# Kernel optimization log

Measured on AMD Instinct MI355X. Metric: run time of the kernel, lower is better.

## Reference

```python
import jax, jax.numpy as jnp
import numpy as np

NUM_EMBEDDINGS = 8192
EMBEDDING_DIM = 256
COMMITMENT_COST = 0.25


def setup_inputs() -> dict:
    key = jax.random.key(0)
    k1, k2 = jax.random.split(key)
    inputs = jax.random.normal(k1, (32, 32, 32, EMBEDDING_DIM), dtype=jnp.float32)
    # flax nn.initializers.uniform(scale=1/num_embeddings) -> U[0, scale)
    embeddings = jax.random.uniform(
        k2, (NUM_EMBEDDINGS, EMBEDDING_DIM), dtype=jnp.float32,
        minval=0.0, maxval=1.0 / NUM_EMBEDDINGS)
    return {"inputs": inputs, "embeddings": embeddings}


def reference(inputs, embeddings):
    flat_input = inputs.reshape(-1, EMBEDDING_DIM)  # [N, D]
    distances = (jnp.sum(flat_input ** 2, axis=1, keepdims=True)
                 - 2.0 * jnp.dot(flat_input, embeddings.T)
                 + jnp.sum(embeddings ** 2, axis=1)[None, :])
    encoding_indices = jnp.argmin(distances, axis=1)  # [N]
    quantized = embeddings[encoding_indices]  # [N, D]

    e_latent_loss = jnp.mean((jax.lax.stop_gradient(quantized) - flat_input) ** 2)
    q_latent_loss = jnp.mean((quantized - jax.lax.stop_gradient(flat_input)) ** 2)
    vq_loss = q_latent_loss + COMMITMENT_COST * e_latent_loss

    # straight-through estimator
    quantized_st = flat_input + jax.lax.stop_gradient(quantized - flat_input)
    quantized_st = quantized_st.reshape(inputs.shape)

    # perplexity via codebook usage histogram (avoids materializing one-hot)
    counts = jnp.zeros((NUM_EMBEDDINGS,), dtype=flat_input.dtype).at[encoding_indices].add(1.0)
    avg_probs = counts / flat_input.shape[0]
    perplexity = jnp.exp(-jnp.sum(avg_probs * jnp.log(avg_probs + 1e-10)))

    return quantized_st, vq_loss, perplexity, encoding_indices
```

## Files before the change

### kernel.cpp

```cpp
#include <hip/hip_runtime.h>
#include <math.h>

#pragma clang fp contract(off)

#define N_ROWS 32768
#define DIM    256
#define K_EMB  8192
#define BCAP   2048
#define NSUB   256

typedef float  f32x4  __attribute__((ext_vector_type(4)));
typedef short  bf16x8 __attribute__((ext_vector_type(8)));

__device__ __forceinline__ void gl_lds16(const uint4* g, uint4* l) {
  __builtin_amdgcn_global_load_lds(
      (const __attribute__((address_space(1))) unsigned int*)g,
      (__attribute__((address_space(3))) unsigned int*)l,
      16, 0, 0);
}

__device__ __forceinline__ unsigned bf_rne(float f) {
  unsigned u = __float_as_uint(f);
  return (u + 0x7fffu + ((u >> 16) & 1u)) >> 16;
}
__device__ __forceinline__ unsigned pack2(float lo, float hi) {
  return bf_rne(lo) | (bf_rne(hi) << 16);
}

__device__ __forceinline__ float np_pw128_sumsq(const float* __restrict__ a) {
  float4 v0 = *(const float4*)(a);
  float4 v1 = *(const float4*)(a + 4);
  float r0 = v0.x*v0.x, r1 = v0.y*v0.y, r2 = v0.z*v0.z, r3 = v0.w*v0.w;
  float r4 = v1.x*v1.x, r5 = v1.y*v1.y, r6 = v1.z*v1.z, r7 = v1.w*v1.w;
  for (int i = 8; i < 128; i += 8) {
    float4 w0 = *(const float4*)(a + i);
    float4 w1 = *(const float4*)(a + i + 4);
    r0 += w0.x*w0.x; r1 += w0.y*w0.y; r2 += w0.z*w0.z; r3 += w0.w*w0.w;
    r4 += w1.x*w1.x; r5 += w1.y*w1.y; r6 += w1.z*w1.z; r7 += w1.w*w1.w;
  }
  return ((r0+r1)+(r2+r3))+((r4+r5)+(r6+r7));
}

__global__ __launch_bounds__(256) void vq_prep(
    const float* __restrict__ X, const float* __restrict__ E,
    float* __restrict__ A, float* __restrict__ C, uint4* __restrict__ Eb,
    unsigned* __restrict__ hist, unsigned* __restrict__ bcnt,
    unsigned* __restrict__ ovf, unsigned long long* __restrict__ best) {
  const int b = blockIdx.x;
  if (b < 1024) {
    int t = b * 256 + threadIdx.x;
    int tile = t >> 6, l = t & 63;
    int cfg = tile >> 3, ks = tile & 7;
    int code = cfg * 16 + (l & 15);
    int k0 = (ks * 4 + (l >> 4)) * 8;
    const float4* src = (const float4*)(E + (size_t)code * DIM + k0);
    float4 a = src[0], bb = src[1];
    uint4 o;
    o.x = pack2(a.x, a.y);  o.y = pack2(a.z, a.w);
    o.z = pack2(bb.x, bb.y); o.w = pack2(bb.z, bb.w);
    Eb[t] = o;
  } else if (b < 1280) {
    int gid = (b - 1024) * 256 + threadIdx.x;
    int row = gid >> 1, half = gid & 1;
    float s = np_pw128_sumsq(X + (size_t)row * DIM + half * 128);
    float o = __shfl_xor(s, 1);
    if (half == 0) A[row] = s + o;
  } else if (b < 1344) {
    int gid = (b - 1280) * 256 + threadIdx.x;
    int row = gid >> 1, half = gid & 1;
    float s = np_pw128_sumsq(E + (size_t)row * DIM + half * 128);
    float o = __shfl_xor(s, 1);
    if (half == 0) C[row] = s + o;
  } else {
    int i = (b - 1344) * 256 + threadIdx.x;
    ovf[i]  = 0u;
    best[i] = ~0ull;
    if (i < K_EMB) hist[i] = 0u;
    if (i < NSUB)  bcnt[i] = 0u;
  }
}

__global__ __launch_bounds__(256)
__attribute__((amdgpu_waves_per_eu(2, 2)))
void vq_mfma_slice(
    const float* __restrict__ X, const uint4* __restrict__ Eb,
    unsigned short* __restrict__ submax_t) {
  __shared__ __align__(16) unsigned short es[2][64 * 256];

  const int tid   = threadIdx.x;
  const int lane  = tid & 63, w = tid >> 6;
  const int lr    = lane & 15, lg = lane >> 4;
  const int wcg   = w & 1;
  const int wxg   = w >> 1;
  const int rb    = blockIdx.x >> 1;
  const int slice = blockIdx.x & 1;
  const int row0  = rb * 128;

  const uint4* ebase = Eb + (size_t)slice * 131072;

#pragma unroll
  for (int i = 0; i < 8; ++i) {
    int u = tid + i * 256;
    gl_lds16(ebase + u, ((uint4*)&es[0][0]) + u);
  }

  bf16x8 bx[4][8];
#pragma unroll
  for (int rf = 0; rf < 4; ++rf) {
    const float* xr = X + (size_t)(row0 + wxg * 64 + rf * 16 + lr) * DIM;
#pragma unroll
    for (int ks = 0; ks < 8; ++ks) {
      int k0 = (ks * 4 + lg) * 8;
      float4 a = *(const float4*)(xr + k0);
      float4 b = *(const float4*)(xr + k0 + 4);
      uint4 o;
      o.x = pack2(a.x, a.y); o.y = pack2(a.z, a.w);
      o.z = pack2(b.x, b.y); o.w = pack2(b.z, b.w);
      bx[rf][ks] = *(bf16x8*)&o;
    }
  }
  __syncthreads();

  for (int c = 0; c < 64; ++c) {
    const int cur = c & 1;
    if (c + 1 < 64) {
#pragma unroll
      for (int i = 0; i < 8; ++i) {
        int u = tid + i * 256;
        gl_lds16(ebase + (size_t)(c + 1) * 2048 + u, ((uint4*)&es[cur ^ 1][0]) + u);
      }
    }

    f32x4 acc[2][4];
#pragma unroll
    for (int ce = 0; ce < 2; ++ce)
#pragma unroll
      for (int rf = 0; rf < 4; ++rf)
        acc[ce][rf] = (f32x4){0.f, 0.f, 0.f, 0.f};

    const unsigned short* eb = &es[cur][0];
    __builtin_amdgcn_s_setprio(1);
#pragma unroll
    for (int ks = 0; ks < 8; ++ks) {
      bf16x8 ev0 = *(const bf16x8*)(eb + (((wcg * 2 + 0) * 8 + ks) * 64 + lane) * 8);
      bf16x8 ev1 = *(const bf16x8*)(eb + (((wcg * 2 + 1) * 8 + ks) * 64 + lane) * 8);
#pragma unroll
      for (int rf = 0; rf < 4; ++rf) {
        acc[0][rf] = __builtin_amdgcn_mfma_f32_16x16x32_bf16(ev0, bx[rf][ks], acc[0][rf], 0, 0, 0);
        acc[1][rf] = __builtin_amdgcn_mfma_f32_16x16x32_bf16(ev1, bx[rf][ks], acc[1][rf], 0, 0, 0);
      }
    }
    __builtin_amdgcn_s_setprio(0);

    const int sub = slice * 128 + c * 2 + wcg;
#pragma unroll
    for (int rf = 0; rf < 4; ++rf) {
      float m = acc[0][rf][0];
#pragma unroll
      for (int ce = 0; ce < 2; ++ce)
#pragma unroll
        for (int rg = 0; rg < 4; ++rg)
          if (ce | rg) m = fmaxf(m, acc[ce][rf][rg]);
      m = fmaxf(m, __shfl_xor(m, 16));
      m = fmaxf(m, __shfl_xor(m, 32));
      if (lg == 0) {
        int qi = (int)((m + 0.0625f) * 524288.0f);
        qi = qi < 0 ? 0 : (qi > 65535 ? 65535 : qi);
        submax_t[(size_t)sub * N_ROWS + row0 + wxg * 64 + rf * 16 + lr] =
            (unsigned short)qi;
      }
    }

    __syncthreads();
  }
}

__global__ __launch_bounds__(256) void vq_flag(
    const unsigned short* __restrict__ submax_t, const float* __restrict__ A,
    unsigned* __restrict__ bcnt, unsigned short* __restrict__ buckets,
    unsigned* __restrict__ ovf) {
  __shared__ unsigned cntA[NSUB], baseS[NSUB], cntC[NSUB];
  const int t   = threadIdx.x;
  const int row = blockIdx.x * 256 + t;
  cntA[t] = 0u; cntC[t] = 0u;
  __syncthreads();

  int mq = 0;
  for (int s = 0; s < NSUB; ++s) {
    int q = submax_t[(size_t)s * N_ROWS + row];
    mq = q > mq ? q : mq;
  }
  const int wq   = (int)((sqrtf(A[row]) * 4e-6f + 9.6e-5f) * 524288.0f) + 2;
  const int thrq = mq - wq;

  for (int s = 0; s < NSUB; ++s)
    if ((int)submax_t[(size_t)s * N_ROWS + row] >= thrq) atomicAdd(&cntA[s], 1u);
  __syncthreads();

  baseS[t] = atomicAdd(&bcnt[t], cntA[t]);
  __syncthreads();

  for (int s = 0; s < NSUB; ++s) {
    if ((int)submax_t[(size_t)s * N_ROWS + row] >= thrq) {
      unsigned p = baseS[s] + atomicAdd(&cntC[s], 1u);
      if (p < BCAP) buckets[s * BCAP + p] = (unsigned short)row;
      else          ovf[row] = 1u;
    }
  }
}

__global__ __launch_bounds__(256) void vq_exact(
    const float* __restrict__ X, const float* __restrict__ E,
    const float* __restrict__ A, const float* __restrict__ C,
    const unsigned* __restrict__ bcnt, const unsigned short* __restrict__ buckets,
    unsigned long long* __restrict__ best) {
  __shared__ float e_lds[32][260];
  __shared__ float xr[4][4][256];
  const int tid  = threadIdx.x;
  const int lane = tid & 63, w = tid >> 6;
  const int bk   = blockIdx.x >> 2, q4 = blockIdx.x & 3;

#pragma unroll
  for (int i = 0; i < 8; ++i) {
    int u = tid + i * 256;
    int code = u >> 6, koff = (u & 63) * 4;
    float4 v = *(const float4*)(E + (size_t)(bk * 32 + code) * DIM + koff);
    *(float4*)(&e_lds[code][koff]) = v;
  }
  __syncthreads();

  int n = (int)bcnt[bk]; if (n > BCAP) n = BCAP;
  const int   half = lane >> 5, c32 = lane & 31;
  const int   j  = bk * 32 + c32;
  const float cj = C[j];

  for (int p0 = q4 * 16 + w * 4; p0 < n; p0 += 64) {
    int valid[4], rows[4];
#pragma unroll
    for (int k = 0; k < 4; ++k) {
      int pk = p0 + k;
      valid[k] = (pk < n);
      rows[k]  = buckets[(size_t)bk * BCAP + (pk < n ? pk : p0)];
    }
#pragma unroll
    for (int k = 0; k < 4; ++k)
      *(float4*)(&xr[w][k][lane * 4]) =
          *(const float4*)(X + (size_t)rows[k] * DIM + lane * 4);
    asm volatile("s_waitcnt lgkmcnt(0)" ::: "memory");

    float acc0 = 0.f, acc1 = 0.f;
    const float* xa = &xr[w][half][0];
    const float* xb = &xr[w][half + 2][0];
#pragma unroll 4
    for (int kq = 0; kq < 64; ++kq) {
      float4 ev = *(const float4*)(&e_lds[c32][kq * 4]);
      float4 x0 = *(const float4*)(xa + kq * 4);
      float4 x1 = *(const float4*)(xb + kq * 4);
      acc0 = fmaf(x0.x, ev.x, acc0); acc0 = fmaf(x0.y, ev.y, acc0);
      acc0 = fmaf(x0.z, ev.z, acc0); acc0 = fmaf(x0.w, ev.w, acc0);
      acc1 = fmaf(x1.x, ev.x, acc1); acc1 = fmaf(x1.y, ev.y, acc1);
      acc1 = fmaf(x1.z, ev.z, acc1); acc1 = fmaf(x1.w, ev.w, acc1);
    }
    float d0 = (A[rows[half]]     - 2.0f * acc0) + cj;
    float d1 = (A[rows[half + 2]] - 2.0f * acc1) + cj;
    int   j0 = j, j1 = j;
#pragma unroll
    for (int mm = 1; mm < 32; mm <<= 1) {
      float od = __shfl_xor(d0, mm); int oj = __shfl_xor(j0, mm);
      if (od < d0 || (od == d0 && oj < j0)) { d0 = od; j0 = oj; }
      od = __shfl_xor(d1, mm); oj = __shfl_xor(j1, mm);
      if (od < d1 || (od == d1 && oj < j1)) { d1 = od; j1 = oj; }
    }
    if (c32 == 0) {
      if (valid[half])
        atomicMin(&best[rows[half]],
                  ((unsigned long long)__float_as_uint(d0) << 32) | (unsigned)j0);
      if (valid[half + 2])
        atomicMin(&best[rows[half + 2]],
                  ((unsigned long long)__float_as_uint(d1) << 32) | (unsigned)j1);
    }
  }
}

__global__ __launch_bounds__(256) void vq_finish(
    const float* __restrict__ X, const float* __restrict__ E,
    const float* __restrict__ A, const float* __restrict__ C,
    const unsigned* __restrict__ ovf, const unsigned long long* __restrict__ best,
    int* __restrict__ idx_out, float* __restrict__ idxf_out) {
  int row  = blockIdx.x * 4 + (threadIdx.x >> 6);
  int lane = threadIdx.x & 63;
  if (!ovf[row]) {
    if (lane == 0) {
      int j = (int)(best[row] & 0xffffffffu);
      idx_out[row]  = j;
      idxf_out[row] = (float)j;
    }
    return;
  }
  const float a_r = A[row];
  const float4* X4 = (const float4*)(X + (size_t)row * DIM);
  float bd = INFINITY; int bj = 0x7fffffff;
  for (int j = lane; j < K_EMB; j += 64) {
    const float4* E4 = (const float4*)(E + (size_t)j * DIM);
    float acc = 0.f;
    for (int kb = 0; kb < 64; ++kb) {
      float4 xv = X4[kb], ev = E4[kb];
      acc = fmaf(xv.x, ev.x, acc); acc = fmaf(xv.y, ev.y, acc);
      acc = fmaf(xv.z, ev.z, acc); acc = fmaf(xv.w, ev.w, acc);
    }
    float d = (a_r - 2.0f * acc) + C[j];
    if (d < bd || (d == bd && j < bj)) { bd = d; bj = j; }
  }
  for (int m = 1; m < 64; m <<= 1) {
    float od = __shfl_xor(bd, m);
    int   oj = __shfl_xor(bj, m);
    if (od < bd || (od == bd && oj < bj)) { bd = od; bj = oj; }
  }
  if (lane == 0) { idx_out[row] = bj; idxf_out[row] = (float)bj; }
}

__global__ __launch_bounds__(256) void vq_argmin(const float* __restrict__ X,
                                                 const float* __restrict__ E,
                                                 const float* __restrict__ A,
                                                 const float* __restrict__ C,
                                                 int* __restrict__ idx_out,
                                                 float* __restrict__ idxf_out) {
  __shared__ float4 xs4[64 * 64];
  const int tid  = threadIdx.x;
  const int rl   = tid >> 2;
  const int cg   = tid & 3;
  const int row0 = blockIdx.x * 64;

  const float4* Xg = (const float4*)(X + (size_t)row0 * DIM);
  for (int it = 0; it < 16; ++it) {
    int f4 = tid + it * 256;
    float4 v = Xg[f4];
    int r = f4 >> 6, kb = f4 & 63;
    xs4[r * 64 + (kb ^ (r & 7))] = v;
  }
  __syncthreads();

  const float a_r = A[row0 + rl];
  const int   swq = rl & 7;
  const float4* xrow = xs4 + rl * 64;

  float bd = INFINITY;
  int   bj = 0x7fffffff;

  for (int tile = 0; tile < K_EMB; tile += 16) {
    const int j0 = tile + cg * 4;
    const float4* e0 = (const float4*)(E + (size_t)(j0 + 0) * DIM);
    const float4* e1 = (const float4*)(E + (size_t)(j0 + 1) * DIM);
    const float4* e2 = (const float4*)(E + (size_t)(j0 + 2) * DIM);
    const float4* e3 = (const float4*)(E + (size_t)(j0 + 3) * DIM);
    float acc0 = 0.f, acc1 = 0.f, acc2 = 0.f, acc3 = 0.f;
#pragma unroll 4
    for (int kb = 0; kb < 64; ++kb) {
      const float4 xv = xrow[kb ^ swq];
      const float4 q0 = e0[kb], q1 = e1[kb], q2 = e2[kb], q3 = e3[kb];
      acc0 = fmaf(xv.x, q0.x, acc0); acc0 = fmaf(xv.y, q0.y, acc0);
      acc0 = fmaf(xv.z, q0.z, acc0); acc0 = fmaf(xv.w, q0.w, acc0);
      acc1 = fmaf(xv.x, q1.x, acc1); acc1 = fmaf(xv.y, q1.y, acc1);
      acc1 = fmaf(xv.z, q1.z, acc1); acc1 = fmaf(xv.w, q1.w, acc1);
      acc2 = fmaf(xv.x, q2.x, acc2); acc2 = fmaf(xv.y, q2.y, acc2);
      acc2 = fmaf(xv.z, q2.z, acc2); acc2 = fmaf(xv.w, q2.w, acc2);
      acc3 = fmaf(xv.x, q3.x, acc3); acc3 = fmaf(xv.y, q3.y, acc3);
      acc3 = fmaf(xv.z, q3.z, acc3); acc3 = fmaf(xv.w, q3.w, acc3);
    }
    const float d0 = (a_r - 2.0f * acc0) + C[j0 + 0];
    const float d1 = (a_r - 2.0f * acc1) + C[j0 + 1];
    const float d2 = (a_r - 2.0f * acc2) + C[j0 + 2];
    const float d3 = (a_r - 2.0f * acc3) + C[j0 + 3];
    if (d0 < bd) { bd = d0; bj = j0 + 0; }
    if (d1 < bd) { bd = d1; bj = j0 + 1; }
    if (d2 < bd) { bd = d2; bj = j0 + 2; }
    if (d3 < bd) { bd = d3; bj = j0 + 3; }
  }
  for (int m = 1; m < 4; m <<= 1) {
    float od = __shfl_xor(bd, m);
    int   oj = __shfl_xor(bj, m);
    if (od < bd || (od == bd && oj < bj)) { bd = od; bj = oj; }
  }
  if (cg == 0) {
    int row = row0 + rl;
    idx_out[row]  = bj;
    idxf_out[row] = (float)bj;
  }
}

__global__ __launch_bounds__(256) void vq_quant(const float* __restrict__ X,
                                                const float* __restrict__ E,
                                                const int* __restrict__ idx,
                                                float* __restrict__ out_qst,
                                                double* __restrict__ partials,
                                                unsigned* __restrict__ hist) {
  int gid  = blockIdx.x * 256 + threadIdx.x;
  int base = gid * 4;
  int row  = base >> 8;
  int k    = base & 255;
  int j    = idx[row];
  if (k == 0) atomicAdd(&hist[j], 1u);
  const float4 xv = *(const float4*)(X + (size_t)base);
  const float4 ev = *(const float4*)(E + (size_t)j * DIM + k);
  float4 o;
  float d0 = ev.x - xv.x, d1 = ev.y - xv.y, d2 = ev.z - xv.z, d3 = ev.w - xv.w;
  o.x = xv.x + d0; o.y = xv.y + d1; o.z = xv.z + d2; o.w = xv.w + d3;
  double s = (double)d0 * d0 + (double)d1 * d1 + (double)d2 * d2 + (double)d3 * d3;
  *(float4*)(out_qst + (size_t)base) = o;

  for (int m = 32; m; m >>= 1) s += __shfl_xor(s, m);
  __shared__ double wsum[4];
  int lane = threadIdx.x & 63, w = threadIdx.x >> 6;
  if (lane == 0) wsum[w] = s;
  __syncthreads();
  if (threadIdx.x == 0)
    partials[blockIdx.x] = (wsum[0] + wsum[1]) + (wsum[2] + wsum[3]);
}

__global__ void vq_zero(unsigned* counts) {
  int i = blockIdx.x * 256 + threadIdx.x;
  if (i < K_EMB) counts[i] = 0u;
}

__global__ __launch_bounds__(256) void vq_scalars(const double* __restrict__ partials,
                                                  const unsigned* __restrict__ counts,
                                                  float* __restrict__ out_loss,
                                                  float* __restrict__ out_perp) {
  __shared__ double red[256];
  int t = threadIdx.x;
  double s = 0.0;
  for (int i = t; i < 8192; i += 256) s += partials[i];
  red[t] = s;
  __syncthreads();
  for (int o = 128; o; o >>= 1) { if (t < o) red[t] += red[t + o]; __syncthreads(); }
  double mse = red[0] / (double)((size_t)N_ROWS * DIM);
  __syncthreads();

  double p = 0.0;
  for (int i = t; i < K_EMB; i += 256) {
    double pr = (double)counts[i] / (double)N_ROWS;
    p += pr * log(pr + 1e-10);
  }
  red[t] = p;
  __syncthreads();
  for (int o = 128; o; o >>= 1) { if (t < o) red[t] += red[t + o]; __syncthreads(); }
  if (t == 0) {
    float m = (float)mse;
    out_loss[0] = m + 0.25f * m;
    out_perp[0] = (float)exp(-red[0]);
  }
}

extern "C" void kernel_launch(void* const* d_in, const int* in_sizes, int n_in,
                              void* d_out, int out_size, void* d_ws, size_t ws_size,
                              hipStream_t stream) {
  const float* X = (const float*)d_in[0];
  const float* E = (const float*)d_in[1];
  float* out  = (float*)d_out;
  float* qst  = out;
  float* loss = out + 8388608;
  float* perp = out + 8388609;
  float* idxf = out + 8388610;

  float*    A        = (float*)d_ws;
  float*    C        = (float*)((char*)d_ws + 131072);
  int*      idx      = (int*)((char*)d_ws + 163840);
  unsigned* hist     = (unsigned*)((char*)d_ws + 294912);
  double*   partials = (double*)((char*)d_ws + 327680);

  if (ws_size >= 22807552) {
    unsigned long long* best = (unsigned long long*)((char*)d_ws + 393216);
    unsigned* ovf          = (unsigned*)((char*)d_ws + 655360);
    unsigned* bcnt         = (unsigned*)((char*)d_ws + 786432);
    unsigned short* bucket = (unsigned short*)((char*)d_ws + 787456);
    uint4*    Eb           = (uint4*)((char*)d_ws + 1836032);
    unsigned short* sm     = (unsigned short*)((char*)d_ws + 6030336);

    vq_prep       <<<1472, 256, 0, stream>>>(X, E, A, C, Eb, hist, bcnt, ovf, best);
    vq_mfma_slice <<<512,  256, 0, stream>>>(X, Eb, sm);
    vq_flag       <<<128,  256, 0, stream>>>(sm, A, bcnt, bucket, ovf);
    vq_exact      <<<1024, 256, 0, stream>>>(X, E, A, C, bcnt, bucket, best);
    vq_finish     <<<8192, 256, 0, stream>>>(X, E, A, C, ovf, best, idx, idxf);
  } else {
    vq_zero   <<<32,  256, 0, stream>>>(hist);
    {
    }
    vq_prep   <<<1472, 256, 0, stream>>>(X, E, A, C,
                 (uint4*)((char*)d_ws + 1836032 < (char*)d_ws + ws_size ?
                          (char*)d_ws + 393216 : (char*)d_ws + 393216),
                 hist,
                 (unsigned*)((char*)d_ws + 294912),
                 (unsigned*)((char*)d_ws + 294912),
                 (unsigned long long*)((char*)d_ws + 327680));
    vq_argmin <<<512, 256, 0, stream>>>(X, E, A, C, idx, idxf);
  }

  vq_quant  <<<8192, 256, 0, stream>>>(X, E, idx, qst, partials, hist);
  vq_scalars<<<1,    256, 0, stream>>>(partials, hist, loss, perp);
}
```

Baseline: 351.9 us.

## Relax MFMA loop barrier, compact finish kernel, split fallback sumsq

Removes s_setprio around the MFMA loop. Replaces the full __syncthreads in the double-buffered slice loop with a partial vmcnt wait plus a raw barrier, so prefetches can stay in flight across the barrier. Changes vq_finish to one thread per row, with wave-cooperative exact search only for overflowed rows found by ballot, which shrinks the launch from 8192 to 128 blocks. Adds a dedicated sumsq kernel for the fallback path. The partial vmcnt wait carries a risk of reading LDS buffers before their loads land.

```diff
diff --git a/kernel.cpp b/kernel.cpp
--- a/kernel.cpp
+++ b/kernel.cpp
@@ -39,6 +39,16 @@
     r4 += w1.x*w1.x; r5 += w1.y*w1.y; r6 += w1.z*w1.z; r7 += w1.w*w1.w;
   }
   return ((r0+r1)+(r2+r3))+((r4+r5)+(r6+r7));
+}
+
+__global__ __launch_bounds__(256) void vq_sumsq(const float* __restrict__ src,
+                                                float* __restrict__ dst, int nrows) {
+  int gid  = blockIdx.x * 256 + threadIdx.x;
+  int row  = gid >> 1, half = gid & 1;
+  if (row >= nrows) return;
+  float s = np_pw128_sumsq(src + (size_t)row * DIM + half * 128);
+  float o = __shfl_xor(s, 1);
+  if (half == 0) dst[row] = s + o;
 }
 
 __global__ __launch_bounds__(256) void vq_prep(
@@ -139,7 +149,6 @@
         acc[ce][rf] = (f32x4){0.f, 0.f, 0.f, 0.f};
 
     const unsigned short* eb = &es[cur][0];
-    __builtin_amdgcn_s_setprio(1);
 #pragma unroll
     for (int ks = 0; ks < 8; ++ks) {
       bf16x8 ev0 = *(const bf16x8*)(eb + (((wcg * 2 + 0) * 8 + ks) * 64 + lane) * 8);
@@ -150,7 +159,6 @@
         acc[1][rf] = __builtin_amdgcn_mfma_f32_16x16x32_bf16(ev1, bx[rf][ks], acc[1][rf], 0, 0, 0);
       }
     }
-    __builtin_amdgcn_s_setprio(0);
 
     const int sub = slice * 128 + c * 2 + wcg;
 #pragma unroll
@@ -171,7 +179,8 @@
       }
     }
 
-    __syncthreads();
+    asm volatile("s_waitcnt vmcnt(4)" ::: "memory");
+    __builtin_amdgcn_s_barrier();
   }
 }
 
@@ -287,36 +296,40 @@
     const float* __restrict__ A, const float* __restrict__ C,
     const unsigned* __restrict__ ovf, const unsigned long long* __restrict__ best,
     int* __restrict__ idx_out, float* __restrict__ idxf_out) {
-  int row  = blockIdx.x * 4 + (threadIdx.x >> 6);
+  int row  = blockIdx.x * 256 + threadIdx.x;
   int lane = threadIdx.x & 63;
-  if (!ovf[row]) {
-    if (lane == 0) {
-      int j = (int)(best[row] & 0xffffffffu);
-      idx_out[row]  = j;
-      idxf_out[row] = (float)j;
-    }
-    return;
-  }
-  const float a_r = A[row];
-  const float4* X4 = (const float4*)(X + (size_t)row * DIM);
-  float bd = INFINITY; int bj = 0x7fffffff;
-  for (int j = lane; j < K_EMB; j += 64) {
-    const float4* E4 = (const float4*)(E + (size_t)j * DIM);
-    float acc = 0.f;
-    for (int kb = 0; kb < 64; ++kb) {
-      float4 xv = X4[kb], ev = E4[kb];
-      acc = fmaf(xv.x, ev.x, acc); acc = fmaf(xv.y, ev.y, acc);
-      acc = fmaf(xv.z, ev.z, acc); acc = fmaf(xv.w, ev.w, acc);
-    }
-    float d = (a_r - 2.0f * acc) + C[j];
-    if (d < bd || (d == bd && j < bj)) { bd = d; bj = j; }
-  }
-  for (int m = 1; m < 64; m <<= 1) {
-    float od = __shfl_xor(bd, m);
-    int   oj = __shfl_xor(bj, m);
-    if (od < bd || (od == bd && oj < bj)) { bd = od; bj = oj; }
-  }
-  if (lane == 0) { idx_out[row] = bj; idxf_out[row] = (float)bj; }
+  unsigned o = ovf[row];
+  if (!o) {
+    int j = (int)(best[row] & 0xffffffffu);
+    idx_out[row]  = j;
+    idxf_out[row] = (float)j;
+  }
+  unsigned long long m = __ballot(o != 0u);
+  while (m) {
+    int src  = __ffsll((long long)m) - 1;
+    int orow = __shfl(row, src);
+    const float a_r = A[orow];
+    const float4* X4 = (const float4*)(X + (size_t)orow * DIM);
+    float bd = INFINITY; int bj = 0x7fffffff;
+    for (int jj = lane; jj < K_EMB; jj += 64) {
+      const float4* E4 = (const float4*)(E + (size_t)jj * DIM);
+      float acc = 0.f;
+      for (int kb = 0; kb < 64; ++kb) {
+        float4 xv = X4[kb], ev = E4[kb];
+        acc = fmaf(xv.x, ev.x, acc); acc = fmaf(xv.y, ev.y, acc);
+        acc = fmaf(xv.z, ev.z, acc); acc = fmaf(xv.w, ev.w, acc);
+      }
+      float d = (a_r - 2.0f * acc) + C[jj];
+      if (d < bd || (d == bd && jj < bj)) { bd = d; bj = jj; }
+    }
+    for (int mm = 1; mm < 64; mm <<= 1) {
+      float od = __shfl_xor(bd, mm);
+      int   oj = __shfl_xor(bj, mm);
+      if (od < bd || (od == bd && oj < bj)) { bd = od; bj = oj; }
+    }
+    if (lane == 0) { idx_out[orow] = bj; idxf_out[orow] = (float)bj; }
+    m &= m - 1;
+  }
 }
 
 __global__ __launch_bounds__(256) void vq_argmin(const float* __restrict__ X,
@@ -480,18 +493,11 @@
     vq_mfma_slice <<<512,  256, 0, stream>>>(X, Eb, sm);
     vq_flag       <<<128,  256, 0, stream>>>(sm, A, bcnt, bucket, ovf);
     vq_exact      <<<1024, 256, 0, stream>>>(X, E, A, C, bcnt, bucket, best);
-    vq_finish     <<<8192, 256, 0, stream>>>(X, E, A, C, ovf, best, idx, idxf);
+    vq_finish     <<<128,  256, 0, stream>>>(X, E, A, C, ovf, best, idx, idxf);
   } else {
     vq_zero   <<<32,  256, 0, stream>>>(hist);
-    {
-    }
-    vq_prep   <<<1472, 256, 0, stream>>>(X, E, A, C,
-                 (uint4*)((char*)d_ws + 1836032 < (char*)d_ws + ws_size ?
-                          (char*)d_ws + 393216 : (char*)d_ws + 393216),
-                 hist,
-                 (unsigned*)((char*)d_ws + 294912),
-                 (unsigned*)((char*)d_ws + 294912),
-                 (unsigned long long*)((char*)d_ws + 327680));
+    vq_sumsq  <<<256, 256, 0, stream>>>(X, A, N_ROWS);
+    vq_sumsq  <<<64,  256, 0, stream>>>(E, C, K_EMB);
     vq_argmin <<<512, 256, 0, stream>>>(X, E, A, C, idx, idxf);
   }
 
```

Result: no change. 345.2 us (-1.9%).
